# Optimization experiments

Measured on AMD Instinct MI355X. Metric: run time of the kernel, lower is better.

## Reference

```python
import jax, jax.numpy as jnp
import numpy as np

G = 4
N = G * G  # 16 nodes

def _edges():
    e = []
    for i in range(G):
        for j in range(G):
            n = i * G + j
            if j + 1 < G:
                e += [[n, n + 1], [n + 1, n]]
            if i + 1 < G:
                e += [[n, n + G], [n + G, n]]
    # PyG GATConv default add_self_loops=True
    e += [[k, k] for k in range(N)]
    a = np.asarray(e, dtype=np.int32)
    return jnp.asarray(a[:, 0]), jnp.asarray(a[:, 1])

SRC, DST = _edges()  # [E]=64 each


def gat_layer(h, W, att_src, att_dst, bias, concat):
    # h: [B, N, Fin]; W: [Fin, H*C]; att_*: [H, C]
    B = h.shape[0]
    H, C = att_src.shape
    x = (h @ W).reshape(B, N, H, C)
    a_s = (x * att_src).sum(-1)  # [B, N, H]
    a_d = (x * att_dst).sum(-1)
    alpha = jax.nn.leaky_relu(a_s[:, SRC] + a_d[:, DST], negative_slope=0.2)  # [B, E, H]
    alpha = jnp.swapaxes(alpha, 0, 1)  # [E, B, H] (segment ops act on axis 0)
    m = jax.ops.segment_max(alpha, DST, num_segments=N)  # [N, B, H]
    ex = jnp.exp(alpha - m[DST])
    s = jax.ops.segment_sum(ex, DST, num_segments=N)
    w = ex / s[DST]  # softmax over incoming edges per dst node
    msg = w[..., None] * jnp.swapaxes(x, 0, 1)[SRC]  # [E, B, H, C]
    agg = jax.ops.segment_sum(msg, DST, num_segments=N)  # [N, B, H, C]
    agg = jnp.swapaxes(agg, 0, 1)  # [B, N, H, C]
    if concat:
        return agg.reshape(B, N, H * C) + bias
    return agg.mean(axis=2) + bias


def layer_norm(x, g, b, eps=1e-5):
    mu = x.mean(-1, keepdims=True)
    var = ((x - mu) ** 2).mean(-1, keepdims=True)
    return (x - mu) * jax.lax.rsqrt(var + eps) * g + b


def setup_inputs() -> dict:
    key = jax.random.key(0)
    ks = iter(jax.random.split(key, 32))
    B, Cin, Hd, Hh, Dout = 8192, 16, 64, 4, 256
    def gl(k, shape, fan_in):
        return jax.random.normal(k, shape, jnp.float32) * (1.0 / np.sqrt(fan_in))
    inp = {
        'x': jax.random.normal(next(ks), (B, Cin, G, G), jnp.float32),
        'w_in': gl(next(ks), (Cin, Hd), Cin),
        'b_in': jnp.zeros((Hd,), jnp.float32),
        # GAT layer 0: 64 -> 4x64 concat
        'w0': gl(next(ks), (Hd, Hh * Hd), Hd),
        'as0': gl(next(ks), (Hh, Hd), Hd), 'ad0': gl(next(ks), (Hh, Hd), Hd),
        'bias0': jnp.zeros((Hh * Hd,), jnp.float32),
        # GAT layer 1: 256 -> 4x64 concat
        'w1': gl(next(ks), (Hh * Hd, Hh * Hd), Hh * Hd),
        'as1': gl(next(ks), (Hh, Hd), Hd), 'ad1': gl(next(ks), (Hh, Hd), Hd),
        'bias1': jnp.zeros((Hh * Hd,), jnp.float32),
        # GAT layer 2: 256 -> 64 (mean over heads)
        'w2': gl(next(ks), (Hh * Hd, Hh * Hd), Hh * Hd),
        'as2': gl(next(ks), (Hh, Hd), Hd), 'ad2': gl(next(ks), (Hh, Hd), Hd),
        'bias2': jnp.zeros((Hd,), jnp.float32),
        # output MLP: 64 -> 128 -> 256, LN+ReLU after each layer
        'mw1': gl(next(ks), (Hd, Dout // 2), Hd), 'mb1': jnp.zeros((Dout // 2,), jnp.float32),
        'g1': jnp.ones((Dout // 2,), jnp.float32), 'be1': jnp.zeros((Dout // 2,), jnp.float32),
        'mw2': gl(next(ks), (Dout // 2, Dout), Dout // 2), 'mb2': jnp.zeros((Dout,), jnp.float32),
        'g2': jnp.ones((Dout,), jnp.float32), 'be2': jnp.zeros((Dout,), jnp.float32),
    }
    return inp


def reference(x, w_in, b_in, w0, as0, ad0, bias0, w1, as1, ad1, bias1,
              w2, as2, ad2, bias2, mw1, mb1, g1, be1, mw2, mb2, g2, be2):
    B = x.shape[0]
    # grid -> node features: (B,C,H,W) -> (B,H,W,C) -> (B,N,C)
    h = jnp.transpose(x, (0, 2, 3, 1)).reshape(B, N, -1)
    h = jax.nn.relu(h @ w_in + b_in)
    h = gat_layer(h, w0, as0, ad0, bias0, concat=True)
    h = jax.nn.relu(h)  # dropout inactive in eval
    h = gat_layer(h, w1, as1, ad1, bias1, concat=True)
    h = jax.nn.relu(h)
    h = gat_layer(h, w2, as2, ad2, bias2, concat=False)  # [B, N, 64]
    gr = h.mean(axis=1)  # global mean pool over the 16 nodes
    y = jax.nn.relu(layer_norm(gr @ mw1 + mb1, g1, be1))
    y = jax.nn.relu(layer_norm(y @ mw2 + mb2, g2, be2))
    return y
```

## Files before the change

kernel.cpp:

```cpp
#include <hip/hip_runtime.h>
#include <hip/hip_bf16.h>

typedef unsigned short u16;
typedef unsigned int   u32;
typedef __attribute__((ext_vector_type(8)))  short bf16x8;
typedef __attribute__((ext_vector_type(16))) float f32x16;

#define GPB 4
#define ZERO16 (f32x16){0.f,0.f,0.f,0.f,0.f,0.f,0.f,0.f,0.f,0.f,0.f,0.f,0.f,0.f,0.f,0.f}
#define MFMA32 __builtin_amdgcn_mfma_f32_32x32x16_bf16

__constant__ int ADJ_DEG[16] = {3,4,4,3, 4,5,5,4, 4,5,5,4, 3,4,4,3};
__constant__ int ADJ_SRC[16][5] = {
  {0,1,4,0,0},   {1,0,2,5,0},   {2,1,3,6,0},   {3,2,7,0,0},
  {4,5,0,8,0},   {5,4,6,1,9},   {6,5,7,2,10},  {7,6,3,11,0},
  {8,9,4,12,0},  {9,8,10,5,13}, {10,9,11,6,14},{11,10,7,15,0},
  {12,13,8,0,0}, {13,12,14,9,0},{14,13,15,10,0},{15,14,11,0,0}
};

struct SMem {
  char hA[64*512];
  char hBT[4*256*32];
  union {
    struct { float asd[64][8]; char ptb[16*16*32]; } post;
    struct { float grs[4][64]; float z1[4][128]; float red[2][8][2]; } mlp;
  } u;
};

__device__ __forceinline__ int swz(int row, int b) { return (row << 9) + (b ^ ((row & 7) << 4)); }
__device__ __forceinline__ int xswz(int g, int c, int b) {
  return (g << 13) + (c << 5) + (b ^ (((c >> 2) & 1) << 4));
}
__device__ __forceinline__ u32 f2bf1(float x) {
  u32 u = __float_as_uint(x);
  return (u + 0x7fffu + ((u >> 16) & 1u)) >> 16;
}
__device__ __forceinline__ u32 pk2(float a, float b) {
  __hip_bfloat162 h2 = __float22bfloat162_rn(make_float2(a, b));
  union { __hip_bfloat162 h; u32 u; } cv; cv.h = h2; return cv.u;
}

template<int KS>
__device__ __forceinline__ void gemm32(SMem& sm, const uint4* __restrict__ wsrc, int t) {
  const int lane = t & 63, w = t >> 6;
  const int l31 = lane & 31, hi = lane >> 5;
  const bool hasAtt = (w < 2);

  f32x16 acc0 = ZERO16, acc1 = ZERO16, accA = ZERO16;

#pragma unroll 4
  for (int ks = 0; ks < KS; ++ks) {
    const uint4 bw = wsrc[(ks*9 + w)*64 + lane];
    uint4 ba;
    if (hasAtt) ba = wsrc[(ks*9 + 8)*64 + lane];
    const bf16x8 a0 = *(const bf16x8*)(sm.hA + swz(l31,      ks*32 + hi*16));
    const bf16x8 a1 = *(const bf16x8*)(sm.hA + swz(32 + l31, ks*32 + hi*16));
    acc0 = MFMA32(a0, *(const bf16x8*)&bw, acc0, 0, 0, 0);
    acc1 = MFMA32(a1, *(const bf16x8*)&bw, acc1, 0, 0, 0);
    if (hasAtt) accA = MFMA32((w == 0) ? a0 : a1, *(const bf16x8*)&ba, accA, 0, 0, 0);
  }

  const int c = w*32 + l31;
#pragma unroll
  for (int mh = 0; mh < 2; ++mh) {
    const f32x16 A = mh ? acc1 : acc0;
#pragma unroll
    for (int grp = 0; grp < 4; ++grp) {
      const int g  = mh*2 + (grp >> 1);
      const int n0 = (grp & 1)*8 + hi*4;
      uint2 o;
      o.x = pk2(A[grp*4+0], A[grp*4+1]);
      o.y = pk2(A[grp*4+2], A[grp*4+3]);
      *(uint2*)(sm.hBT + xswz(g, c, n0*2)) = o;
    }
  }

  if (hasAtt) {
    if (l31 < 8) {
#pragma unroll
      for (int grp = 0; grp < 4; ++grp) {
        const int g  = w*2 + (grp >> 1);
        const int n0 = (grp & 1)*8 + hi*4;
#pragma unroll
        for (int i = 0; i < 4; ++i)
          sm.u.post.asd[g*16 + n0 + i][l31] = accA[grp*4+i];
      }
    }
    const int g = w*2 + hi;
    const int h = lane & 3;
#pragma unroll
    for (int dd = 0; dd < 2; ++dd) {
      const int d = ((lane >> 2) & 7) + dd*8;
      const int deg = ADJ_DEG[d];
      const float advl = sm.u.post.asd[g*16 + d][4 + h];
      float al[5]; int srcs[5];
      float m = -1e30f;
#pragma unroll
      for (int k = 0; k < 5; ++k) {
        srcs[k] = (k < deg) ? ADJ_SRC[d][k] : 99;
        float v = 0.f;
        if (k < deg) {
          v = sm.u.post.asd[g*16 + srcs[k]][h] + advl;
          v = (v > 0.f) ? v : 0.2f * v;
          m = fmaxf(m, v);
        }
        al[k] = v;
      }
      float ssum = 0.f;
#pragma unroll
      for (int k = 0; k < 5; ++k)
        if (k < deg) { const float e = __expf(al[k] - m); al[k] = e; ssum += e; }
      const float inv = 1.f / ssum;
      float p[16];
#pragma unroll
      for (int s = 0; s < 16; ++s) {
        float v = 0.f;
#pragma unroll
        for (int k = 0; k < 5; ++k) v = (srcs[k] == s) ? al[k] * inv : v;
        p[s] = v;
      }
      uint4 lo, hh;
      lo.x = pk2(p[0],p[1]);   lo.y = pk2(p[2],p[3]);   lo.z = pk2(p[4],p[5]);   lo.w = pk2(p[6],p[7]);
      hh.x = pk2(p[8],p[9]);   hh.y = pk2(p[10],p[11]); hh.z = pk2(p[12],p[13]); hh.w = pk2(p[14],p[15]);
      char* pt = sm.u.post.ptb + (((g*4 + h)*16 + d) << 5);
      *(uint4*)pt = lo;
      *(uint4*)(pt + 16) = hh;
    }
  }
}

template<int MODE>
__device__ __forceinline__ void agg32(SMem& sm, const float* __restrict__ bias, int t) {
  const int lane = t & 63, w = t >> 6;
  const int l31 = lane & 31, hi = lane >> 5;
  const int g = w >> 1;
  const bf16x8 zero8 = {0,0,0,0,0,0,0,0};

  if (MODE == 0) {
#pragma unroll
    for (int i = 0; i < 4; ++i) {
      const int mt = (w & 1)*4 + i;
      const int h = mt >> 1;
      bf16x8 pb = zero8;
      if (l31 < 16)
        pb = *(const bf16x8*)(sm.u.post.ptb + (((g*4 + h)*16 + l31) << 5) + hi*16);
      const bf16x8 a = *(const bf16x8*)(sm.hBT + xswz(g, mt*32 + l31, hi*16));
      f32x16 acc = ZERO16;
      acc = MFMA32(a, pb, acc, 0, 0, 0);
      if (l31 < 16) {
        const int row = g*16 + l31;
#pragma unroll
        for (int grp = 0; grp < 4; ++grp) {
          const int cb = mt*32 + grp*8 + hi*4;
          const float4 bv = *(const float4*)(bias + cb);
          uint2 o;
          o.x = pk2(fmaxf(acc[grp*4+0] + bv.x, 0.f), fmaxf(acc[grp*4+1] + bv.y, 0.f));
          o.y = pk2(fmaxf(acc[grp*4+2] + bv.z, 0.f), fmaxf(acc[grp*4+3] + bv.w, 0.f));
          *(uint2*)(sm.hA + swz(row, 2*cb)) = o;
        }
      }
    }
  } else {
    const int mt = w & 1;
    f32x16 acc = ZERO16;
#pragma unroll
    for (int h = 0; h < 4; ++h) {
      bf16x8 pb = zero8;
      if (l31 < 16)
        pb = *(const bf16x8*)(sm.u.post.ptb + (((g*4 + h)*16 + l31) << 5) + hi*16);
      const bf16x8 a = *(const bf16x8*)(sm.hBT + xswz(g, h*64 + mt*32 + l31, hi*16));
      acc = MFMA32(a, pb, acc, 0, 0, 0);
    }
    if (l31 < 16) {
      float (*o64)[68] = (float (*)[68])sm.hA;
      const int row = g*16 + l31;
#pragma unroll
      for (int grp = 0; grp < 4; ++grp) {
        const int cb = mt*32 + grp*8 + hi*4;
        const float4 bv = *(const float4*)(bias + cb);
        float4 ov;
        ov.x = fmaf(0.25f, acc[grp*4+0], bv.x);
        ov.y = fmaf(0.25f, acc[grp*4+1], bv.y);
        ov.z = fmaf(0.25f, acc[grp*4+2], bv.z);
        ov.w = fmaf(0.25f, acc[grp*4+3], bv.w);
        *(float4*)&o64[row][cb] = ov;
      }
    }
  }
}

extern "C" __global__ void __launch_bounds__(512, 4)
gat_main(const float* __restrict__ xg, const float* __restrict__ b_in,
         const float* __restrict__ bias0, const float* __restrict__ bias1,
         const float* __restrict__ bias2,
         const uint4* __restrict__ wq0, const uint4* __restrict__ wq1,
         const uint4* __restrict__ wq2, const uint4* __restrict__ winq,
         const float* __restrict__ mw1, const float* __restrict__ mb1,
         const float* __restrict__ g1, const float* __restrict__ be1,
         const u32* __restrict__ mwb2, const float* __restrict__ mb2,
         const float* __restrict__ g2, const float* __restrict__ be2,
         float* __restrict__ out, int Btot)
{
  __shared__ SMem sm;
  const int t = threadIdx.x;
  const int b0 = blockIdx.x * GPB;
  if (b0 >= Btot) return;
  const int lane = t & 63, w = t >> 6;
  const int l31 = lane & 31, hi = lane >> 5;

  if (w < 4) {
    const int mtC = w & 1, ntN = w >> 1;
    const int gg = ntN*2 + (l31 >> 4), node = l31 & 15;
    float xv[8];
#pragma unroll
    for (int j = 0; j < 8; ++j)
      xv[j] = xg[(size_t)(b0 + gg)*256 + (hi*8 + j)*16 + node];
    union { u32 uu[4]; bf16x8 v; } bcv;
#pragma unroll
    for (int j = 0; j < 4; ++j) bcv.uu[j] = pk2(xv[2*j], xv[2*j+1]);
    const uint4 aw4 = winq[mtC*64 + lane];
    f32x16 acc = ZERO16;
    acc = MFMA32(*(const bf16x8*)&aw4, bcv.v, acc, 0, 0, 0);
    const int row = ntN*32 + l31;
#pragma unroll
    for (int grp = 0; grp < 4; ++grp) {
      const int cb = mtC*32 + grp*8 + hi*4;
      const float4 bv = *(const float4*)(b_in + cb);
      uint2 o;
      o.x = pk2(fmaxf(acc[grp*4+0] + bv.x, 0.f), fmaxf(acc[grp*4+1] + bv.y, 0.f));
      o.y = pk2(fmaxf(acc[grp*4+2] + bv.z, 0.f), fmaxf(acc[grp*4+3] + bv.w, 0.f));
      *(uint2*)(sm.hA + swz(row, 2*cb)) = o;
    }
  }
  __syncthreads();

  gemm32<4>(sm, wq0, t);   __syncthreads();
  agg32<0>(sm, bias0, t);  __syncthreads();

  gemm32<16>(sm, wq1, t);  __syncthreads();
  agg32<0>(sm, bias1, t);  __syncthreads();

  gemm32<16>(sm, wq2, t);  __syncthreads();
  agg32<1>(sm, bias2, t);  __syncthreads();

  if (t < 256) {
    const int g = t >> 6, col = t & 63;
    const float (*o64)[68] = (const float (*)[68])sm.hA;
    float s = 0.f;
#pragma unroll
    for (int r = 0; r < 16; ++r) s += o64[(g << 4) + r][col];
    sm.u.mlp.grs[g][col] = s * (1.f/16.f);
  }
  __syncthreads();

  const int mg = t >> 7, o = t & 127;
  float a1v = mb1[o];
#pragma unroll 8
  for (int k = 0; k < 64; ++k) a1v = fmaf(sm.u.mlp.grs[mg][k], mw1[k*128 + o], a1v);
  {
    float su = a1v, sq = a1v*a1v;
#pragma unroll
    for (int off = 32; off >= 1; off >>= 1) { su += __shfl_xor(su, off); sq += __shfl_xor(sq, off); }
    if (lane == 0) { sm.u.mlp.red[0][w][0] = su; sm.u.mlp.red[0][w][1] = sq; }
  }
  __syncthreads();
  {
    const float mu = (sm.u.mlp.red[0][2*mg][0] + sm.u.mlp.red[0][2*mg+1][0]) * (1.f/128.f);
    const float mq = (sm.u.mlp.red[0][2*mg][1] + sm.u.mlp.red[0][2*mg+1][1]) * (1.f/128.f);
    const float rstd = rsqrtf(mq - mu*mu + 1e-5f);
    sm.u.mlp.z1[mg][o] = fmaxf((a1v - mu)*rstd*g1[o] + be1[o], 0.f);
  }
  __syncthreads();

  {
    const float2 bb2 = *(const float2*)(mb2 + 2*o);
    float c0 = bb2.x, c1 = bb2.y;
#pragma unroll 8
    for (int k = 0; k < 128; ++k) {
      const float zk = sm.u.mlp.z1[mg][k];
      const u32 uw = mwb2[k*128 + o];
      c0 = fmaf(zk, __uint_as_float(uw << 16), c0);
      c1 = fmaf(zk, __uint_as_float(uw & 0xffff0000u), c1);
    }
    float su = c0 + c1, sq = c0*c0 + c1*c1;
#pragma unroll
    for (int off = 32; off >= 1; off >>= 1) { su += __shfl_xor(su, off); sq += __shfl_xor(sq, off); }
    if (lane == 0) { sm.u.mlp.red[1][w][0] = su; sm.u.mlp.red[1][w][1] = sq; }
    __syncthreads();
    const float mu = (sm.u.mlp.red[1][2*mg][0] + sm.u.mlp.red[1][2*mg+1][0]) * (1.f/256.f);
    const float mq = (sm.u.mlp.red[1][2*mg][1] + sm.u.mlp.red[1][2*mg+1][1]) * (1.f/256.f);
    const float rstd = rsqrtf(mq - mu*mu + 1e-5f);
    const float2 gg2  = *(const float2*)(g2  + 2*o);
    const float2 bbe2 = *(const float2*)(be2 + 2*o);
    float2 ov;
    ov.x = fmaxf((c0 - mu)*rstd*gg2.x + bbe2.x, 0.f);
    ov.y = fmaxf((c1 - mu)*rstd*gg2.y + bbe2.y, 0.f);
    *(float2*)(out + (size_t)(b0 + mg)*256 + 2*o) = ov;
  }
}

__global__ void __launch_bounds__(256)
prep_w(const float* __restrict__ w0, const float* __restrict__ as0, const float* __restrict__ ad0,
       const float* __restrict__ w1, const float* __restrict__ as1, const float* __restrict__ ad1,
       const float* __restrict__ w2, const float* __restrict__ as2, const float* __restrict__ ad2,
       const float* __restrict__ w_in, const float* __restrict__ mw2, u16* __restrict__ wf) {
  const int f = blockIdx.x*256 + threadIdx.x;
  if (f >= 199680) return;
  if (f >= 166912) { wf[f] = (u16)f2bf1(mw2[f - 166912]); return; }
  if (f >= 165888) {
    const int local = f - 165888;
    const int nt = local >> 9, lane = (local >> 3) & 63, j = local & 7;
    wf[f] = (u16)f2bf1(w_in[((lane >> 5)*8 + j)*64 + nt*32 + (lane & 31)]);
    return;
  }
  const float *W, *as_, *ad_; int local;
  if (f < 18432)      { W = w0; as_ = as0; ad_ = ad0; local = f; }
  else if (f < 92160) { W = w1; as_ = as1; ad_ = ad1; local = f - 18432; }
  else                { W = w2; as_ = as2; ad_ = ad2; local = f - 92160; }
  const int ks = local / 4608;
  const int r  = local - ks*4608;
  const int nt = r >> 9;
  const int lane = (r >> 3) & 63;
  const int j = r & 7;
  const int k = ks*16 + (lane >> 5)*8 + j;
  const int col = lane & 31;
  float val;
  if (nt < 8) {
    val = W[k*256 + nt*32 + col];
  } else if (col < 8) {
    const int h = col & 3;
    const float* av = (col < 4) ? as_ : ad_;
    float s = 0.f;
    for (int c = 0; c < 64; ++c) s = fmaf(W[k*256 + h*64 + c], av[h*64 + c], s);
    val = s;
  } else {
    val = 0.f;
  }
  wf[f] = (u16)f2bf1(val);
}

extern "C" void kernel_launch(void* const* d_in, const int* in_sizes, int n_in,
                              void* d_out, int out_size, void* d_ws, size_t ws_size,
                              hipStream_t stream) {
  (void)n_in; (void)out_size; (void)ws_size;
  const float* xg   = (const float*)d_in[0];
  const float* w_in = (const float*)d_in[1];
  const float* b_in = (const float*)d_in[2];
  const float* w0   = (const float*)d_in[3];
  const float* as0  = (const float*)d_in[4];
  const float* ad0  = (const float*)d_in[5];
  const float* bi0  = (const float*)d_in[6];
  const float* w1   = (const float*)d_in[7];
  const float* as1  = (const float*)d_in[8];
  const float* ad1  = (const float*)d_in[9];
  const float* bi1  = (const float*)d_in[10];
  const float* w2   = (const float*)d_in[11];
  const float* as2  = (const float*)d_in[12];
  const float* ad2  = (const float*)d_in[13];
  const float* bi2  = (const float*)d_in[14];
  const float* mw1  = (const float*)d_in[15];
  const float* mb1  = (const float*)d_in[16];
  const float* g1   = (const float*)d_in[17];
  const float* be1  = (const float*)d_in[18];
  const float* mw2  = (const float*)d_in[19];
  const float* mb2  = (const float*)d_in[20];
  const float* g2   = (const float*)d_in[21];
  const float* be2  = (const float*)d_in[22];
  float* out = (float*)d_out;

  const int Btot = in_sizes[0] / 256;
  u16* wf = (u16*)d_ws;
  const uint4* wq0  = (const uint4*)wf;
  const uint4* wq1  = (const uint4*)(wf + 18432);
  const uint4* wq2  = (const uint4*)(wf + 92160);
  const uint4* winq = (const uint4*)(wf + 165888);
  const u32*   mwb2 = (const u32*)(wf + 166912);

  hipLaunchKernelGGL(prep_w, dim3(780), dim3(256), 0, stream,
                     w0, as0, ad0, w1, as1, ad1, w2, as2, ad2, w_in, mw2, wf);

  const int nblocks = (Btot + GPB - 1) / GPB;
  hipLaunchKernelGGL(gat_main, dim3(nblocks), dim3(512), 0, stream,
                     xg, b_in, bi0, bi1, bi2, wq0, wq1, wq2, winq,
                     mw1, mb1, g1, be1, mwb2, mb2, g2, be2, out, Btot);
}
```

Before: 171.4 us.

## Swizzle LDS layouts, prefetch weights, and fuse mean-pool into final aggregation

Adds extra XOR terms to the hA, hBT and attention-probability LDS address swizzles to spread accesses across more banks, and splits some hBT reads into two 8-byte loads. The GEMM weight fetch becomes software-pipelined: the next k-step's weights load while the current MFMAs run. The final GAT aggregation now reduces over the 16 nodes with wave shuffles and writes the pooled vector directly, which removes the separate pooling pass and one barrier. The costs are extra XOR address math, more registers for the prefetched weights, and 64 shuffles per wave in the last stage.

```diff
diff --git a/kernel.cpp b/kernel.cpp
--- a/kernel.cpp
+++ b/kernel.cpp
@@ -27,9 +27,14 @@
   } u;
 };
 
-__device__ __forceinline__ int swz(int row, int b) { return (row << 9) + (b ^ ((row & 7) << 4)); }
+__device__ __forceinline__ int swz(int row, int b) {
+  return (row << 9) + (b ^ ((row & 7) << 4) ^ (((row >> 3) & 1) << 5));
+}
 __device__ __forceinline__ int xswz(int g, int c, int b) {
-  return (g << 13) + (c << 5) + (b ^ (((c >> 2) & 1) << 4));
+  return (g << 13) + (c << 5) + (b ^ (((c >> 2) & 1) << 4) ^ (((c >> 3) & 1) << 3));
+}
+__device__ __forceinline__ int ptbx(int g, int h, int d, int b) {
+  return (((g*4 + h)*16 + d) << 5) + (b ^ (((h ^ (d >> 2)) & 1) << 4));
 }
 __device__ __forceinline__ u32 f2bf1(float x) {
   u32 u = __float_as_uint(x);
@@ -38,6 +43,12 @@
 __device__ __forceinline__ u32 pk2(float a, float b) {
   __hip_bfloat162 h2 = __float22bfloat162_rn(make_float2(a, b));
   union { __hip_bfloat162 h; u32 u; } cv; cv.h = h2; return cv.u;
+}
+__device__ __forceinline__ bf16x8 hbt_read(const SMem& sm, int g, int c, int hi) {
+  union { uint2 u2[2]; bf16x8 v; } cv;
+  cv.u2[0] = *(const uint2*)(sm.hBT + xswz(g, c, hi*16));
+  cv.u2[1] = *(const uint2*)(sm.hBT + xswz(g, c, hi*16 + 8));
+  return cv.v;
 }
 
 template<int KS>
@@ -48,16 +59,23 @@
 
   f32x16 acc0 = ZERO16, acc1 = ZERO16, accA = ZERO16;
 
-#pragma unroll 4
+  uint4 bw = wsrc[w*64 + lane];
+  uint4 ba;
+  if (hasAtt) ba = wsrc[8*64 + lane];
+
+#pragma unroll
   for (int ks = 0; ks < KS; ++ks) {
-    const uint4 bw = wsrc[(ks*9 + w)*64 + lane];
-    uint4 ba;
-    if (hasAtt) ba = wsrc[(ks*9 + 8)*64 + lane];
+    uint4 bwn, ban;
+    if (ks + 1 < KS) {
+      bwn = wsrc[((ks+1)*9 + w)*64 + lane];
+      if (hasAtt) ban = wsrc[((ks+1)*9 + 8)*64 + lane];
+    }
     const bf16x8 a0 = *(const bf16x8*)(sm.hA + swz(l31,      ks*32 + hi*16));
     const bf16x8 a1 = *(const bf16x8*)(sm.hA + swz(32 + l31, ks*32 + hi*16));
     acc0 = MFMA32(a0, *(const bf16x8*)&bw, acc0, 0, 0, 0);
     acc1 = MFMA32(a1, *(const bf16x8*)&bw, acc1, 0, 0, 0);
     if (hasAtt) accA = MFMA32((w == 0) ? a0 : a1, *(const bf16x8*)&ba, accA, 0, 0, 0);
+    if (ks + 1 < KS) { bw = bwn; if (hasAtt) ba = ban; }
   }
 
   const int c = w*32 + l31;
@@ -122,9 +140,8 @@
       uint4 lo, hh;
       lo.x = pk2(p[0],p[1]);   lo.y = pk2(p[2],p[3]);   lo.z = pk2(p[4],p[5]);   lo.w = pk2(p[6],p[7]);
       hh.x = pk2(p[8],p[9]);   hh.y = pk2(p[10],p[11]); hh.z = pk2(p[12],p[13]); hh.w = pk2(p[14],p[15]);
-      char* pt = sm.u.post.ptb + (((g*4 + h)*16 + d) << 5);
-      *(uint4*)pt = lo;
-      *(uint4*)(pt + 16) = hh;
+      *(uint4*)(sm.u.post.ptb + ptbx(g, h, d, 0))  = lo;
+      *(uint4*)(sm.u.post.ptb + ptbx(g, h, d, 16)) = hh;
     }
   }
 }
@@ -143,8 +160,8 @@
       const int h = mt >> 1;
       bf16x8 pb = zero8;
       if (l31 < 16)
-        pb = *(const bf16x8*)(sm.u.post.ptb + (((g*4 + h)*16 + l31) << 5) + hi*16);
-      const bf16x8 a = *(const bf16x8*)(sm.hBT + xswz(g, mt*32 + l31, hi*16));
+        pb = *(const bf16x8*)(sm.u.post.ptb + ptbx(g, h, l31, hi*16));
+      const bf16x8 a = hbt_read(sm, g, mt*32 + l31, hi);
       f32x16 acc = ZERO16;
       acc = MFMA32(a, pb, acc, 0, 0, 0);
       if (l31 < 16) {
@@ -167,24 +184,30 @@
     for (int h = 0; h < 4; ++h) {
       bf16x8 pb = zero8;
       if (l31 < 16)
-        pb = *(const bf16x8*)(sm.u.post.ptb + (((g*4 + h)*16 + l31) << 5) + hi*16);
-      const bf16x8 a = *(const bf16x8*)(sm.hBT + xswz(g, h*64 + mt*32 + l31, hi*16));
+        pb = *(const bf16x8*)(sm.u.post.ptb + ptbx(g, h, l31, hi*16));
+      const bf16x8 a = hbt_read(sm, g, h*64 + mt*32 + l31, hi);
       acc = MFMA32(a, pb, acc, 0, 0, 0);
     }
-    if (l31 < 16) {
-      float (*o64)[68] = (float (*)[68])sm.hA;
-      const int row = g*16 + l31;
-#pragma unroll
-      for (int grp = 0; grp < 4; ++grp) {
-        const int cb = mt*32 + grp*8 + hi*4;
-        const float4 bv = *(const float4*)(bias + cb);
-        float4 ov;
-        ov.x = fmaf(0.25f, acc[grp*4+0], bv.x);
-        ov.y = fmaf(0.25f, acc[grp*4+1], bv.y);
-        ov.z = fmaf(0.25f, acc[grp*4+2], bv.z);
-        ov.w = fmaf(0.25f, acc[grp*4+3], bv.w);
-        *(float4*)&o64[row][cb] = ov;
-      }
+#pragma unroll
+    for (int i = 0; i < 16; ++i) {
+      acc[i] += __shfl_xor(acc[i], 1);
+      acc[i] += __shfl_xor(acc[i], 2);
+      acc[i] += __shfl_xor(acc[i], 4);
+      acc[i] += __shfl_xor(acc[i], 8);
+    }
+    if (l31 < 4) {
+      float4 ov;
+      if (l31 == 0)      { ov.x = acc[0];  ov.y = acc[1];  ov.z = acc[2];  ov.w = acc[3];  }
+      else if (l31 == 1) { ov.x = acc[4];  ov.y = acc[5];  ov.z = acc[6];  ov.w = acc[7];  }
+      else if (l31 == 2) { ov.x = acc[8];  ov.y = acc[9];  ov.z = acc[10]; ov.w = acc[11]; }
+      else               { ov.x = acc[12]; ov.y = acc[13]; ov.z = acc[14]; ov.w = acc[15]; }
+      const int c0 = mt*32 + l31*8 + hi*4;
+      const float4 bv = *(const float4*)(bias + c0);
+      ov.x = fmaf(1.f/64.f, ov.x, bv.x);
+      ov.y = fmaf(1.f/64.f, ov.y, bv.y);
+      ov.z = fmaf(1.f/64.f, ov.z, bv.z);
+      ov.w = fmaf(1.f/64.f, ov.w, bv.w);
+      *(float4*)&sm.u.mlp.grs[g][c0] = ov;
     }
   }
 }
@@ -242,16 +265,6 @@
 
   gemm32<16>(sm, wq2, t);  __syncthreads();
   agg32<1>(sm, bias2, t);  __syncthreads();
-
-  if (t < 256) {
-    const int g = t >> 6, col = t & 63;
-    const float (*o64)[68] = (const float (*)[68])sm.hA;
-    float s = 0.f;
-#pragma unroll
-    for (int r = 0; r < 16; ++r) s += o64[(g << 4) + r][col];
-    sm.u.mlp.grs[g][col] = s * (1.f/16.f);
-  }
-  __syncthreads();
 
   const int mg = t >> 7, o = t & 127;
   float a1v = mb1[o];
```

After: 176.2 us. 2.8% more time.
